# Optimization experiments

Measured on AMD Instinct MI355X. Metric: run time of the kernel, lower is better.

Reference implementation:

```python
import jax, jax.numpy as jnp
import numpy as np

N_NODES, N_EDGES, BATCH = 50000, 100000, 256
H = 64            # dim_hidden_features
D_NODE, D_EDGE, D_RBF = 110, 8, 8
D_SET = 2 * H     # Set2Set input_dim = 128, output_dim = 256
D_HID = 512
D_CAT = 54
MP_STEPS, S2S_ITERS = 4, 3


def setup_inputs() -> dict:
    key = jax.random.key(0)
    ks = iter(jax.random.split(key, 48))

    def nrm(shape, s=0.05):
        return jax.random.normal(next(ks), shape, dtype=jnp.float32) * s

    inp = {}
    inp["node_attribute"] = jax.random.normal(next(ks), (N_NODES, D_NODE), dtype=jnp.float32)
    inp["edge_attribute"] = jax.random.normal(next(ks), (N_EDGES, D_EDGE), dtype=jnp.float32)
    inp["edge_length"] = jax.random.uniform(next(ks), (N_EDGES,), dtype=jnp.float32)
    inp["src"] = jax.random.randint(next(ks), (N_EDGES,), 0, N_NODES, dtype=jnp.int32)
    inp["dst"] = jax.random.randint(next(ks), (N_EDGES,), 0, N_NODES, dtype=jnp.int32)
    inp["node_graph"] = jnp.sort(jax.random.randint(next(ks), (N_NODES,), 0, BATCH, dtype=jnp.int32))
    # atom_feature_projector
    inp["proj_W"] = nrm((D_NODE, H)); inp["proj_b"] = jnp.zeros((H,), jnp.float32)
    # RBF layer: centers ~ U(0,1), beta = 10 (per reset_parameters)
    inp["centers"] = jax.random.uniform(next(ks), (D_RBF,), dtype=jnp.float32)
    inp["beta"] = jnp.full((D_RBF,), 10.0, jnp.float32)
    # NNConv edge function: Linear(16 -> 64*64), plus NNConv bias
    inp["bond_W"] = nrm((D_EDGE + D_RBF, H * H)); inp["bond_b"] = jnp.zeros((H * H,), jnp.float32)
    inp["conv_b"] = jnp.zeros((H,), jnp.float32)
    # GRU (input H, hidden H); PyTorch layout (3H, in)
    inp["gru_Wih"] = nrm((3 * H, H)); inp["gru_Whh"] = nrm((3 * H, H))
    inp["gru_bih"] = jnp.zeros((3 * H,), jnp.float32); inp["gru_bhh"] = jnp.zeros((3 * H,), jnp.float32)
    # Set2Set LSTM: input 2*D_SET=256, hidden D_SET=128, 2 layers; PyTorch layout (4H, in)
    inp["lstm_Wih0"] = nrm((4 * D_SET, 2 * D_SET)); inp["lstm_Whh0"] = nrm((4 * D_SET, D_SET))
    inp["lstm_bih0"] = jnp.zeros((4 * D_SET,), jnp.float32); inp["lstm_bhh0"] = jnp.zeros((4 * D_SET,), jnp.float32)
    inp["lstm_Wih1"] = nrm((4 * D_SET, D_SET)); inp["lstm_Whh1"] = nrm((4 * D_SET, D_SET))
    inp["lstm_bih1"] = jnp.zeros((4 * D_SET,), jnp.float32); inp["lstm_bhh1"] = jnp.zeros((4 * D_SET,), jnp.float32)
    # sparsify: Linear(256 -> 512) + PReLU(init 0.25)
    inp["sp_W"] = nrm((2 * D_SET, D_HID)); inp["sp_b"] = jnp.zeros((D_HID,), jnp.float32)
    inp["prelu_a"] = jnp.array([0.25], jnp.float32)
    # catalyst1 head: hiddens[0] (512->512 ReLU, 512->512 Tanh) then outputs[0] (512->54)
    inp["h0_W1"] = nrm((D_HID, D_HID)); inp["h0_b1"] = jnp.zeros((D_HID,), jnp.float32)
    inp["h0_W2"] = nrm((D_HID, D_HID)); inp["h0_b2"] = jnp.zeros((D_HID,), jnp.float32)
    inp["out_W"] = nrm((D_HID, D_CAT)); inp["out_b"] = jnp.zeros((D_CAT,), jnp.float32)
    return inp


def _lstm_cell(x, h, c, Wih, Whh, bih, bhh):
    # PyTorch LSTM gate order: i, f, g, o
    g = x @ Wih.T + bih + h @ Whh.T + bhh
    i, f, gg, o = jnp.split(g, 4, axis=-1)
    c = jax.nn.sigmoid(f) * c + jax.nn.sigmoid(i) * jnp.tanh(gg)
    h = jax.nn.sigmoid(o) * jnp.tanh(c)
    return h, c


def reference(node_attribute, edge_attribute, edge_length, src, dst, node_graph,
              proj_W, proj_b, centers, beta, bond_W, bond_b, conv_b,
              gru_Wih, gru_Whh, gru_bih, gru_bhh,
              lstm_Wih0, lstm_Whh0, lstm_bih0, lstm_bhh0,
              lstm_Wih1, lstm_Whh1, lstm_bih1, lstm_bhh1,
              sp_W, sp_b, prelu_a, h0_W1, h0_b1, h0_W2, h0_b2, out_W, out_b):
    n_nodes = node_attribute.shape[0]
    # atom feature projection
    x = jax.nn.relu(node_attribute @ proj_W + proj_b)                       # (N, H)
    # edge features = [edge_attribute, RBF(length)]
    rbf = jnp.exp(-beta * (edge_length[:, None] - centers[None, :]) ** 2)   # (E, 8)
    efeat = jnp.concatenate([edge_attribute, rbf], axis=-1)                 # (E, 16)
    # NNConv per-edge weight matrix; edge features are constant over MP steps
    W_e = (efeat @ bond_W + bond_b).reshape(-1, H, H)                       # (E, H, H)

    feat, h = x, x
    for _ in range(MP_STEPS):
        # NNConv: message = h_src @ W_e, sum-aggregated at dst, plus bias
        m = jnp.einsum('ei,eio->eo', feat[src], W_e)                        # (E, H)
        agg = jax.ops.segment_sum(m, dst, num_segments=n_nodes) + conv_b    # (N, H)
        gx = jax.nn.relu(agg)
        # GRU cell (PyTorch gate order r, z, n)
        gi = gx @ gru_Wih.T + gru_bih
        gh = h @ gru_Whh.T + gru_bhh
        i_r, i_z, i_n = jnp.split(gi, 3, axis=-1)
        h_r, h_z, h_n = jnp.split(gh, 3, axis=-1)
        r = jax.nn.sigmoid(i_r + h_r)
        z = jax.nn.sigmoid(i_z + h_z)
        n = jnp.tanh(i_n + r * h_n)
        h = (1.0 - z) * n + z * h
        feat = h
    node_agg = jnp.concatenate([feat, x], axis=-1)                          # (N, 2H)

    # Set2Set pooling over graphs (segment softmax attention, 2-layer LSTM)
    B = BATCH
    h0 = c0 = jnp.zeros((B, D_SET), node_agg.dtype)
    h1 = c1 = jnp.zeros((B, D_SET), node_agg.dtype)
    q_star = jnp.zeros((B, 2 * D_SET), node_agg.dtype)
    for _ in range(S2S_ITERS):
        h0, c0 = _lstm_cell(q_star, h0, c0, lstm_Wih0, lstm_Whh0, lstm_bih0, lstm_bhh0)
        h1, c1 = _lstm_cell(h0, h1, c1, lstm_Wih1, lstm_Whh1, lstm_bih1, lstm_bhh1)
        q = h1                                                              # (B, 128)
        e = jnp.sum(node_agg * q[node_graph], axis=-1)                      # (N,)
        emax = jax.ops.segment_max(e, node_graph, num_segments=B)
        p = jnp.exp(e - emax[node_graph])
        denom = jax.ops.segment_sum(p, node_graph, num_segments=B)
        alpha = p / denom[node_graph]                                       # per-graph softmax
        r_out = jax.ops.segment_sum(node_agg * alpha[:, None], node_graph, num_segments=B)
        q_star = jnp.concatenate([q, r_out], axis=-1)                       # (B, 256)

    # sparsify (Linear + PReLU)
    feats = q_star @ sp_W + sp_b                                            # (B, 512)
    feats = jnp.where(feats >= 0, feats, prelu_a * feats)
    # catalyst1 head
    hid = jnp.tanh(jax.nn.relu(feats @ h0_W1 + h0_b1) @ h0_W2 + h0_b2)
    return jax.nn.softmax(hid @ out_W + out_b, axis=-1)                     # (B, 54)
```

## Files before the change

kernel.cpp:

```cpp
#include <hip/hip_runtime.h>
#include <math.h>

constexpr int N = 50000;
constexpr int E = 100000;
constexpr int B = 256;
constexpr int H = 64;
constexpr int DN = 110;

#define DEV __device__ __forceinline__

typedef __attribute__((ext_vector_type(8))) short short8;
typedef __attribute__((ext_vector_type(4))) float floatx4;

DEV float sigf(float x) { return 1.0f / (1.0f + expf(-x)); }

DEV short f2bf(float f) {
    unsigned u = __float_as_uint(f);
    unsigned r = (u + 0x7fffu + ((u >> 16) & 1u)) >> 16;
    return (short)r;
}
DEV float bf2f(short s) { return __uint_as_float(((unsigned)(unsigned short)s) << 16); }

DEV void cvt8(const float* p, short8& hi, short8& lo) {
    float4 u0 = *(const float4*)p;
    float4 u1 = *(const float4*)(p + 4);
    float vv[8] = {u0.x, u0.y, u0.z, u0.w, u1.x, u1.y, u1.z, u1.w};
#pragma unroll
    for (int j = 0; j < 8; ++j) {
        short hb = f2bf(vv[j]);
        hi[j] = hb;
        lo[j] = f2bf(vv[j] - bf2f(hb));
    }
}

__global__ void k_izero(int* p, int n) {
    int i = blockIdx.x * 256 + threadIdx.x;
    if (i < n) p[i] = 0;
}

DEV void d_transpose(const float* in, float* out, int R, int C, int idx) {
    int r = idx / C, c = idx % C;
    out[c * R + r] = in[idx];
}

DEV void d_prepB(const float* __restrict__ W, short* __restrict__ out,
                 int NT16, int ld, int trans, int ocap, int idx) {
    int lane = idx & 63;
    int t = idx >> 6;
    int ntile = t % NT16;
    int kt = t / NT16;
    int quad = lane >> 4, col = lane & 15;
    int o = ntile * 16 + col;
    short hi[8], lo[8];
#pragma unroll
    for (int j = 0; j < 8; ++j) {
        int k = kt * 32 + quad * 8 + j;
        float v = 0.0f;
        if (o < ocap) v = trans ? W[(size_t)o * ld + k] : W[(size_t)k * ld + o];
        short hb = f2bf(v);
        hi[j] = hb;
        lo[j] = f2bf(v - bf2f(hb));
    }
    short* dh = out + (((size_t)(t * 2 + 0) * 64 + lane) * 8);
    short* dl = out + (((size_t)(t * 2 + 1) * 64 + lane) * 8);
#pragma unroll
    for (int j = 0; j < 8; ++j) { dh[j] = hi[j]; dl[j] = lo[j]; }
}

DEV void d_prepW(const float* __restrict__ bond_W, const float* __restrict__ bond_b,
                 short* __restrict__ wf, int idx) {
    int lane = idx & 63;
    int t = idx >> 6;
    int ks = t & 1;
    int nt = (t >> 1) & 3;
    int kk = t >> 3;
    const float* S = (kk < 16) ? (bond_W + kk * 4096) : bond_b;
    int quad = lane >> 4, col = lane & 15;
    short hi[8], lo[8];
#pragma unroll
    for (int j = 0; j < 8; ++j) {
        int i = ks * 32 + quad * 8 + j;
        float v = S[i * 64 + nt * 16 + col];
        short hb = f2bf(v);
        hi[j] = hb;
        lo[j] = f2bf(v - bf2f(hb));
    }
    short* dh = wf + (((size_t)(t * 2 + 0) * 64 + lane) * 8);
    short* dl = wf + (((size_t)(t * 2 + 1) * 64 + lane) * 8);
#pragma unroll
    for (int j = 0; j < 8; ++j) { dh[j] = hi[j]; dl[j] = lo[j]; }
}

__launch_bounds__(256)
__global__ void k_prep0(const float* lWih0, const float* lWhh0, const float* lWih1, const float* lWhh1,
                        float* lW0T, float* lU0T, float* lW1T, float* lU1T,
                        const float* bond_W, const float* bond_b, short* wf,
                        const float* gru_Wih, const float* gru_Whh, short* fgI, short* fgH,
                        float* zreg) {
    int idx = blockIdx.x * 256 + threadIdx.x;
    if (idx < 131072) { d_transpose(lWih0, lW0T, 512, 256, idx); return; }
    idx -= 131072;
    if (idx < 65536) { d_transpose(lWhh0, lU0T, 512, 128, idx); return; }
    idx -= 65536;
    if (idx < 65536) { d_transpose(lWih1, lW1T, 512, 128, idx); return; }
    idx -= 65536;
    if (idx < 65536) { d_transpose(lWhh1, lU1T, 512, 128, idx); return; }
    idx -= 65536;
    if (idx < 8704) { d_prepW(bond_W, bond_b, wf, idx); return; }
    idx -= 8704;
    if (idx < 1536) { d_prepB(gru_Wih, fgI, 12, 64, 1, 192, idx); return; }
    idx -= 1536;
    if (idx < 1536) { d_prepB(gru_Whh, fgH, 12, 64, 1, 192, idx); return; }
    idx -= 1536;
    if (idx < 196608) { zreg[idx] = 0.0f; return; }
}
constexpr int PREP0_TOTAL = 131072 + 3 * 65536 + 8704 + 2 * 1536 + 196608;

__launch_bounds__(256)
__global__ void k_prephead(const float* sp_W, short* fsp, const float* h0_W1, short* fw1,
                           const float* h0_W2, short* fw2, const float* out_W, short* fow) {
    int idx = blockIdx.x * 256 + threadIdx.x;
    if (idx < 16384) { d_prepB(sp_W, fsp, 32, 512, 0, 512, idx); return; }
    idx -= 16384;
    if (idx < 32768) { d_prepB(h0_W1, fw1, 32, 512, 0, 512, idx); return; }
    idx -= 32768;
    if (idx < 32768) { d_prepB(h0_W2, fw2, 32, 512, 0, 512, idx); return; }
    idx -= 32768;
    if (idx < 4096) { d_prepB(out_W, fow, 4, 54, 0, 54, idx); return; }
}
constexpr int PREPH_TOTAL = 16384 + 2 * 32768 + 4096;

__global__ void k_deg(const int* __restrict__ dst, int* __restrict__ deg) {
    int e = blockIdx.x * 256 + threadIdx.x;
    if (e < E) atomicAdd(&deg[dst[e]], 1);
}
__global__ void k_scan1(const int* __restrict__ deg, int* __restrict__ bsum) {
    __shared__ int s[256];
    int b = blockIdx.x, tid = threadIdx.x;
    int idx = b * 256 + tid;
    s[tid] = (idx < N) ? deg[idx] : 0;
    __syncthreads();
    for (int st = 128; st > 0; st >>= 1) {
        if (tid < st) s[tid] += s[tid + st];
        __syncthreads();
    }
    if (tid == 0) bsum[b] = s[0];
}
__global__ void k_scan2p(int* __restrict__ bsum, int nb) {
    __shared__ int s[256];
    int tid = threadIdx.x;
    int v = (tid < nb) ? bsum[tid] : 0;
    s[tid] = v;
    __syncthreads();
    for (int off = 1; off < 256; off <<= 1) {
        int t = (tid >= off) ? s[tid - off] : 0;
        __syncthreads();
        s[tid] += t;
        __syncthreads();
    }
    if (tid < nb) bsum[tid] = s[tid] - v;
}
__global__ void k_scan3(const int* __restrict__ deg, const int* __restrict__ bsum,
                        int* __restrict__ cursor, int* __restrict__ roff) {
    __shared__ int s[256];
    int b = blockIdx.x, tid = threadIdx.x;
    int idx = b * 256 + tid;
    int v = (idx < N) ? deg[idx] : 0;
    s[tid] = v;
    __syncthreads();
    for (int off = 1; off < 256; off <<= 1) {
        int t = (tid >= off) ? s[tid - off] : 0;
        __syncthreads();
        s[tid] += t;
        __syncthreads();
    }
    if (idx < N) {
        int start = bsum[b] + s[tid] - v;
        cursor[idx] = start;
        roff[idx] = start;
    }
    if (idx == 0) roff[N] = E;
}
__global__ void k_scat(const int* __restrict__ src, const int* __restrict__ dst,
                       int* __restrict__ cursor, int* __restrict__ srcp,
                       int* __restrict__ epos) {
    int e = blockIdx.x * 256 + threadIdx.x;
    if (e >= E) return;
    int d = dst[e];
    int pos = atomicAdd(&cursor[d], 1);
    srcp[pos] = src[e];
    epos[e] = pos;
}

__launch_bounds__(256)
__global__ void k_proj(const float* __restrict__ na, const float* __restrict__ W,
                       const float* __restrict__ b, float* __restrict__ x,
                       short* __restrict__ hs) {
    __shared__ float Ws[DN * 64];
    __shared__ float as[16][112];
    int tid = threadIdx.x;
    for (int i = tid; i < DN * 64; i += 256) Ws[i] = W[i];
    int n0 = blockIdx.x * 16;
    for (int i = tid; i < 16 * DN; i += 256) {
        int nn = i / DN, ii = i % DN;
        as[nn][ii] = na[(n0 + nn) * DN + ii];
    }
    __syncthreads();
    int o = tid & 63, ng = tid >> 6;
    float bo = b[o];
    for (int j = 0; j < 4; ++j) {
        int nn = ng * 4 + j;
        float acc = bo;
#pragma unroll 10
        for (int i = 0; i < DN; ++i) acc += as[nn][i] * Ws[i * 64 + o];
        float v = fmaxf(acc, 0.0f);
        int n = n0 + nn;
        x[(size_t)n * 64 + o] = v;
        short hb = f2bf(v);
        hs[(size_t)n * 128 + o] = hb;
        hs[(size_t)n * 128 + 64 + o] = f2bf(v - bf2f(hb));
    }
}

__global__ void k_efeat2(const float* __restrict__ ea, const float* __restrict__ el,
                         const float* __restrict__ centers, const float* __restrict__ beta,
                         const int* __restrict__ epos, float* __restrict__ ef_t) {
    int e = blockIdx.x * 256 + threadIdx.x;
    if (e >= E) return;
    int pos = epos[e];
    float L = el[e];
#pragma unroll
    for (int j = 0; j < 8; ++j) ef_t[j * E + pos] = ea[e * 8 + j];
#pragma unroll
    for (int j = 0; j < 8; ++j) {
        float d = L - centers[j];
        ef_t[(8 + j) * E + pos] = expf(-beta[j] * d * d);
    }
    ef_t[16 * E + pos] = 1.0f;
}

__launch_bounds__(256)
__global__ void k_msg8(const short* __restrict__ hs, const float* __restrict__ ef_t,
                       const short* __restrict__ wf, const int* __restrict__ srcp,
                       float* __restrict__ m) {
    __shared__ float efs[17 * 64];
    __shared__ int srcs[64];

    int tid = threadIdx.x;
    int e0 = blockIdx.x * 64;
    int lane = tid & 63;
    int nt = tid >> 6;
    int quad = lane >> 4, col = lane & 15;

    if (tid < 64) {
        int eg = e0 + tid;
        srcs[tid] = (eg < E) ? srcp[eg] : 0;
    }
    for (int i = tid; i < 17 * 64; i += 256) {
        int kk = i >> 6, e = i & 63;
        int eg = e0 + e;
        efs[i] = (eg < E) ? ef_t[(size_t)kk * E + eg] : 0.0f;
    }
    __syncthreads();

    short8 Ah[4][2], Al[4][2];
#pragma unroll
    for (int mt = 0; mt < 4; ++mt) {
        int s = srcs[mt * 16 + col];
        const short* hp = hs + (size_t)s * 128 + quad * 8;
#pragma unroll
        for (int ks = 0; ks < 2; ++ks) {
            Ah[mt][ks] = *(const short8*)(hp + ks * 32);
            Al[mt][ks] = *(const short8*)(hp + 64 + ks * 32);
        }
    }

    const short8* Wf = (const short8*)wf;
    float C[4][4] = {};

#define LOADB(d0, d1, d2, d3, KK)                      \
    {                                                  \
        int tb_ = ((KK) * 4 + nt) * 2;                 \
        d0 = Wf[((tb_ + 0) * 2 + 0) * 64 + lane];      \
        d1 = Wf[((tb_ + 1) * 2 + 0) * 64 + lane];      \
        d2 = Wf[((tb_ + 0) * 2 + 1) * 64 + lane];      \
        d3 = Wf[((tb_ + 1) * 2 + 1) * 64 + lane];      \
    }

    short8 c0, c1, c2, c3, n0_, n1_, n2_, n3_, q0, q1, q2, q3;
    LOADB(c0, c1, c2, c3, 0);
    LOADB(n0_, n1_, n2_, n3_, 1);
    LOADB(q0, q1, q2, q3, 2);

#pragma unroll 1
    for (int kk = 0; kk < 17; ++kk) {
        int kn = kk + 3;
        if (kn > 16) kn = 16;
        short8 p0, p1, p2, p3;
        LOADB(p0, p1, p2, p3, kn);

#pragma unroll
        for (int mt = 0; mt < 4; ++mt) {
            floatx4 T = {0.0f, 0.0f, 0.0f, 0.0f};
            T = __builtin_amdgcn_mfma_f32_16x16x32_bf16(Ah[mt][0], c0, T, 0, 0, 0);
            T = __builtin_amdgcn_mfma_f32_16x16x32_bf16(Ah[mt][1], c1, T, 0, 0, 0);
            T = __builtin_amdgcn_mfma_f32_16x16x32_bf16(Al[mt][0], c0, T, 0, 0, 0);
            T = __builtin_amdgcn_mfma_f32_16x16x32_bf16(Al[mt][1], c1, T, 0, 0, 0);
            T = __builtin_amdgcn_mfma_f32_16x16x32_bf16(Ah[mt][0], c2, T, 0, 0, 0);
            T = __builtin_amdgcn_mfma_f32_16x16x32_bf16(Ah[mt][1], c3, T, 0, 0, 0);
            float4 ef = *(const float4*)&efs[kk * 64 + mt * 16 + quad * 4];
            C[mt][0] += ef.x * T[0];
            C[mt][1] += ef.y * T[1];
            C[mt][2] += ef.z * T[2];
            C[mt][3] += ef.w * T[3];
        }
        c0 = n0_; c1 = n1_; c2 = n2_; c3 = n3_;
        n0_ = q0; n1_ = q1; n2_ = q2; n3_ = q3;
        q0 = p0; q1 = p1; q2 = p2; q3 = p3;
    }
#undef LOADB

    int o = nt * 16 + col;
#pragma unroll
    for (int mt = 0; mt < 4; ++mt) {
#pragma unroll
        for (int r = 0; r < 4; ++r) {
            int eg = e0 + mt * 16 + quad * 4 + r;
            if (eg < E) m[(size_t)eg * 64 + o] = C[mt][r];
        }
    }
}

__launch_bounds__(256)
__global__ void k_gru3(const float* __restrict__ m, const int* __restrict__ roff,
                       const float* __restrict__ conv_b, short* __restrict__ hs,
                       const short* __restrict__ fI, const short* __restrict__ fH,
                       const float* __restrict__ bih, const float* __restrict__ bhh) {
    int tid = threadIdx.x, lane = tid & 63, nt = tid >> 6;
    int quad = lane >> 4, col = lane & 15;
    int n0 = blockIdx.x * 32;

    short8 Gh[2][2], Gl[2][2], Hh[2][2], Hl[2][2];
#pragma unroll
    for (int mt = 0; mt < 2; ++mt) {
        int node = n0 + mt * 16 + col;
        bool ok = node < N;
        int nc = ok ? node : (N - 1);
        int rs = roff[nc];
        int re = ok ? roff[nc + 1] : rs;
        float acc[2][8];
#pragma unroll
        for (int ks = 0; ks < 2; ++ks) {
            const float* cb = conv_b + ks * 32 + quad * 8;
#pragma unroll
            for (int j = 0; j < 8; ++j) acc[ks][j] = cb[j];
        }
        for (int r = rs; r < re; ++r) {
            const float* mp = m + (size_t)r * 64 + quad * 8;
            float4 a0 = *(const float4*)mp;
            float4 a1 = *(const float4*)(mp + 4);
            float4 b0 = *(const float4*)(mp + 32);
            float4 b1 = *(const float4*)(mp + 36);
            acc[0][0] += a0.x; acc[0][1] += a0.y; acc[0][2] += a0.z; acc[0][3] += a0.w;
            acc[0][4] += a1.x; acc[0][5] += a1.y; acc[0][6] += a1.z; acc[0][7] += a1.w;
            acc[1][0] += b0.x; acc[1][1] += b0.y; acc[1][2] += b0.z; acc[1][3] += b0.w;
            acc[1][4] += b1.x; acc[1][5] += b1.y; acc[1][6] += b1.z; acc[1][7] += b1.w;
        }
        const short* hp = hs + (size_t)nc * 128 + quad * 8;
#pragma unroll
        for (int ks = 0; ks < 2; ++ks) {
            short8 hh8 = *(const short8*)(hp + ks * 32);
            short8 hl8 = *(const short8*)(hp + 64 + ks * 32);
            Hh[mt][ks] = hh8;
            Hl[mt][ks] = hl8;
#pragma unroll
            for (int j = 0; j < 8; ++j) {
                float g = ok ? fmaxf(acc[ks][j], 0.0f) : 0.0f;
                short gb = f2bf(g);
                Gh[mt][ks][j] = gb;
                Gl[mt][ks][j] = f2bf(g - bf2f(gb));
            }
        }
        if (!ok) {
#pragma unroll
            for (int ks = 0; ks < 2; ++ks) {
                Hh[mt][ks] = short8{0,0,0,0,0,0,0,0};
                Hl[mt][ks] = short8{0,0,0,0,0,0,0,0};
            }
        }
    }
    __syncthreads();

    const short8* FI = (const short8*)fI;
    const short8* FH = (const short8*)fH;
    floatx4 aI[2][3] = {}, aH[2][3] = {};
#pragma unroll
    for (int ks = 0; ks < 2; ++ks) {
        short8 bIh[3], bIl[3], bHh[3], bHl[3];
#pragma unroll
        for (int g = 0; g < 3; ++g) {
            int t = ks * 12 + g * 4 + nt;
            bIh[g] = FI[(t * 2 + 0) * 64 + lane];
            bIl[g] = FI[(t * 2 + 1) * 64 + lane];
            bHh[g] = FH[(t * 2 + 0) * 64 + lane];
            bHl[g] = FH[(t * 2 + 1) * 64 + lane];
        }
#pragma unroll
        for (int mt = 0; mt < 2; ++mt) {
#pragma unroll
            for (int g = 0; g < 3; ++g) {
                aI[mt][g] = __builtin_amdgcn_mfma_f32_16x16x32_bf16(Gh[mt][ks], bIh[g], aI[mt][g], 0, 0, 0);
                aI[mt][g] = __builtin_amdgcn_mfma_f32_16x16x32_bf16(Gl[mt][ks], bIh[g], aI[mt][g], 0, 0, 0);
                aI[mt][g] = __builtin_amdgcn_mfma_f32_16x16x32_bf16(Gh[mt][ks], bIl[g], aI[mt][g], 0, 0, 0);
                aH[mt][g] = __builtin_amdgcn_mfma_f32_16x16x32_bf16(Hh[mt][ks], bHh[g], aH[mt][g], 0, 0, 0);
                aH[mt][g] = __builtin_amdgcn_mfma_f32_16x16x32_bf16(Hl[mt][ks], bHh[g], aH[mt][g], 0, 0, 0);
                aH[mt][g] = __builtin_amdgcn_mfma_f32_16x16x32_bf16(Hh[mt][ks], bHl[g], aH[mt][g], 0, 0, 0);
            }
        }
    }

    int o = nt * 16 + col;
    float br = bih[o], bz = bih[64 + o], bn = bih[128 + o];
    float cr = bhh[o], cz = bhh[64 + o], cn = bhh[128 + o];
#pragma unroll
    for (int mt = 0; mt < 2; ++mt) {
#pragma unroll
        for (int r = 0; r < 4; ++r) {
            int node = n0 + mt * 16 + quad * 4 + r;
            if (node >= N) continue;
            float rg = sigf(aI[mt][0][r] + br + aH[mt][0][r] + cr);
            float z  = sigf(aI[mt][1][r] + bz + aH[mt][1][r] + cz);
            float ng = tanhf(aI[mt][2][r] + bn + rg * (aH[mt][2][r] + cn));
            size_t hb_ = (size_t)node * 128 + o;
            float hold = bf2f(hs[hb_]) + bf2f(hs[hb_ + 64]);
            float hn = (1.0f - z) * ng + z * hold;
            short hi = f2bf(hn);
            hs[hb_] = hi;
            hs[hb_ + 64] = f2bf(hn - bf2f(hi));
        }
    }
}

__global__ void k_bounds2(const int* __restrict__ ng, int* __restrict__ gs, int* __restrict__ ge) {
    int n = blockIdx.x * 256 + threadIdx.x;
    if (n >= N) return;
    int g = ng[n];
    int gp = (n == 0) ? -1 : ng[n - 1];
    if (g != gp) {
        gs[g] = n;
        if (n > 0) ge[gp] = n;
        for (int q = gp + 1; q < g; ++q) { gs[q] = 0; ge[q] = 0; }
    }
    if (n == N - 1) {
        ge[g] = N;
        for (int q = g + 1; q < B; ++q) { gs[q] = 0; ge[q] = 0; }
    }
}

__launch_bounds__(256)
__global__ void k_s2s(float* __restrict__ h0, float* __restrict__ c0,
                      float* __restrict__ h1, float* __restrict__ c1,
                      float* __restrict__ q_star,
                      const float* __restrict__ W0T, const float* __restrict__ U0T,
                      const float* __restrict__ b0i, const float* __restrict__ b0h,
                      const float* __restrict__ W1T, const float* __restrict__ U1T,
                      const float* __restrict__ b1i, const float* __restrict__ b1h,
                      const short* __restrict__ hs, const float* __restrict__ x,
                      const int* __restrict__ gs, const int* __restrict__ ge) {
    __shared__ float xb[256], hb[128], gb[512], h0n[128], qv[128];
    __shared__ float mrg[4][2][64];
    __shared__ float ml[4][2];
    int g = blockIdx.x, tid = threadIdx.x;
    xb[tid] = q_star[g * 256 + tid];
    if (tid < 128) hb[tid] = h0[g * 128 + tid];
    __syncthreads();
    float g0 = b0i[tid] + b0h[tid];
    float g1 = b0i[tid + 256] + b0h[tid + 256];
    for (int i = 0; i < 256; ++i) {
        float xx = xb[i];
        g0 += xx * W0T[i * 512 + tid];
        g1 += xx * W0T[i * 512 + tid + 256];
    }
    for (int i = 0; i < 128; ++i) {
        float hh = hb[i];
        g0 += hh * U0T[i * 512 + tid];
        g1 += hh * U0T[i * 512 + tid + 256];
    }
    gb[tid] = g0; gb[tid + 256] = g1;
    __syncthreads();
    if (tid < 128) {
        float ii = gb[tid], ff = gb[128 + tid], gg = gb[256 + tid], oo = gb[384 + tid];
        float c = sigf(ff) * c0[g * 128 + tid] + sigf(ii) * tanhf(gg);
        float hn = sigf(oo) * tanhf(c);
        c0[g * 128 + tid] = c; h0[g * 128 + tid] = hn; h0n[tid] = hn;
        hb[tid] = h1[g * 128 + tid];
    }
    __syncthreads();
    float ga = b1i[tid] + b1h[tid];
    float gbv = b1i[tid + 256] + b1h[tid + 256];
    for (int i = 0; i < 128; ++i) {
        float xx = h0n[i], hh = hb[i];
        ga  += xx * W1T[i * 512 + tid]       + hh * U1T[i * 512 + tid];
        gbv += xx * W1T[i * 512 + tid + 256] + hh * U1T[i * 512 + tid + 256];
    }
    gb[tid] = ga; gb[tid + 256] = gbv;
    __syncthreads();
    if (tid < 128) {
        float ii = gb[tid], ff = gb[128 + tid], gg = gb[256 + tid], oo = gb[384 + tid];
        float c = sigf(ff) * c1[g * 128 + tid] + sigf(ii) * tanhf(gg);
        float hn = sigf(oo) * tanhf(c);
        c1[g * 128 + tid] = c; h1[g * 128 + tid] = hn;
        q_star[g * 256 + tid] = hn;
        qv[tid] = hn;
    }
    __syncthreads();
    int s0v = gs[g], s1v = ge[g];
    int lane = tid & 63, grp = tid >> 6;
    float qh = qv[lane], qx = qv[64 + lane];
    float mM = -INFINITY, lL = 0.0f, nh = 0.0f, nx = 0.0f;
    for (int n = s0v + grp; n < s1v; n += 16) {
        float hv[4], xv[4], e[4];
#pragma unroll
// ... 86 lines not shown
    __shared__ float sm[16][64];
    __shared__ float smax[16], sinv[16];
    int tid = threadIdx.x, lane = tid & 63, nt = tid >> 6;
    int quad = lane >> 4, col = lane & 15;
    int s0 = blockIdx.x * 16;
    const short8* F = (const short8*)Bf;
    floatx4 T = {0.0f, 0.0f, 0.0f, 0.0f};
    const float* ap = A + (size_t)(s0 + col) * 512 + quad * 8;
#pragma unroll 4
    for (int kt = 0; kt < 16; ++kt) {
        short8 ah, al;
        cvt8(ap + kt * 32, ah, al);
        int t = kt * 4 + nt;
        short8 bh = F[(t * 2 + 0) * 64 + lane];
        short8 bl = F[(t * 2 + 1) * 64 + lane];
        T = __builtin_amdgcn_mfma_f32_16x16x32_bf16(ah, bh, T, 0, 0, 0);
        T = __builtin_amdgcn_mfma_f32_16x16x32_bf16(al, bh, T, 0, 0, 0);
        T = __builtin_amdgcn_mfma_f32_16x16x32_bf16(ah, bl, T, 0, 0, 0);
    }
    int o = nt * 16 + col;
    float b = (o < 54) ? ob[o] : 0.0f;
#pragma unroll
    for (int r = 0; r < 4; ++r)
        sm[quad * 4 + r][o] = (o < 54) ? (T[r] + b) : -1e30f;
    __syncthreads();
    if (tid < 16) {
        float m = -INFINITY;
        for (int j = 0; j < 54; ++j) m = fmaxf(m, sm[tid][j]);
        float s = 0.0f;
        for (int j = 0; j < 54; ++j) s += expf(sm[tid][j] - m);
        smax[tid] = m;
        sinv[tid] = 1.0f / s;
    }
    __syncthreads();
    for (int idx = tid; idx < 16 * 54; idx += 256) {
        int srow = idx / 54, oo = idx % 54;
        out[(size_t)(s0 + srow) * 54 + oo] = expf(sm[srow][oo] - smax[srow]) * sinv[srow];
    }
}

extern "C" void kernel_launch(void* const* d_in, const int* in_sizes, int n_in,
                              void* d_out, int out_size, void* d_ws, size_t ws_size,
                              hipStream_t stream) {
    const float* node_attr = (const float*)d_in[0];
    const float* edge_attr = (const float*)d_in[1];
    const float* edge_len  = (const float*)d_in[2];
    const int*   src       = (const int*)d_in[3];
    const int*   dst       = (const int*)d_in[4];
    const int*   node_grph = (const int*)d_in[5];
    const float* proj_W    = (const float*)d_in[6];
    const float* proj_b    = (const float*)d_in[7];
    const float* centers   = (const float*)d_in[8];
    const float* beta      = (const float*)d_in[9];
    const float* bond_W    = (const float*)d_in[10];
    const float* bond_b    = (const float*)d_in[11];
    const float* conv_b    = (const float*)d_in[12];
    const float* gru_Wih   = (const float*)d_in[13];
    const float* gru_Whh   = (const float*)d_in[14];
    const float* gru_bih   = (const float*)d_in[15];
    const float* gru_bhh   = (const float*)d_in[16];
    const float* lWih0     = (const float*)d_in[17];
    const float* lWhh0     = (const float*)d_in[18];
    const float* lbih0     = (const float*)d_in[19];
    const float* lbhh0     = (const float*)d_in[20];
    const float* lWih1     = (const float*)d_in[21];
    const float* lWhh1     = (const float*)d_in[22];
    const float* lbih1     = (const float*)d_in[23];
    const float* lbhh1     = (const float*)d_in[24];
    const float* sp_W      = (const float*)d_in[25];
    const float* sp_b      = (const float*)d_in[26];
    const float* prelu_a   = (const float*)d_in[27];
    const float* h0_W1     = (const float*)d_in[28];
    const float* h0_b1     = (const float*)d_in[29];
    const float* h0_W2     = (const float*)d_in[30];
    const float* h0_b2     = (const float*)d_in[31];
    const float* out_W     = (const float*)d_in[32];
    const float* out_b     = (const float*)d_in[33];
    float* out = (float*)d_out;

    float* ws = (float*)d_ws;
    size_t off = 0;
    float* x      = ws + off; off += (size_t)N * 64;
    float* hsf    = ws + off; off += (size_t)N * 64;
    float* ef_t   = ws + off; off += (size_t)E * 17;
    float* m      = ws + off; off += (size_t)E * 64;
    float* wfrag  = ws + off; off += 17 * 16 * 64 * 8 / 2;
    float* fgI    = ws + off; off += 2 * 64 * 192 / 2;
    float* fgH    = ws + off; off += 2 * 64 * 192 / 2;
    float* lW0T   = ws + off; off += 256 * 512;
    float* lU0T   = ws + off; off += 128 * 512;
    float* lW1T   = ws + off; off += 128 * 512;
    float* lU1T   = ws + off; off += 128 * 512;
    float* h0     = ws + off; off += B * 128;
    float* c0     = ws + off; off += B * 128;
    float* h1     = ws + off; off += B * 128;
    float* c1     = ws + off; off += B * 128;
    float* q_star = ws + off; off += B * 256;
    int* gs       = (int*)(ws + off); off += B;
    int* ge       = (int*)(ws + off); off += B;
    int* deg      = (int*)(ws + off); off += N;
    int* cursor   = (int*)(ws + off); off += N;
    int* roff     = (int*)(ws + off); off += N + 1;
    int* bsum     = (int*)(ws + off); off += 256;
    int* srcp     = (int*)(ws + off); off += E;
    int* epos     = (int*)(ws + off); off += E;

    short* hs = (short*)hsf;

    short* fsp = (short*)ef_t;
    short* fw1 = (short*)(ef_t + 131072);
    short* fw2 = (short*)(ef_t + 131072 + 262144);
    short* fow = (short*)(ef_t + 131072 + 2 * 262144);
    float* hb1 = ef_t + 131072 + 2 * 262144 + 32768;
    float* hb2 = hb1 + 131072;

    constexpr int NB = (N + 255) / 256;

    k_izero<<<NB, 256, 0, stream>>>(deg, N);
    k_deg<<<(E + 255) / 256, 256, 0, stream>>>(dst, deg);
    k_scan1<<<NB, 256, 0, stream>>>(deg, bsum);
    k_scan2p<<<1, 256, 0, stream>>>(bsum, NB);
    k_scan3<<<NB, 256, 0, stream>>>(deg, bsum, cursor, roff);
    k_scat<<<(E + 255) / 256, 256, 0, stream>>>(src, dst, cursor, srcp, epos);

    k_prep0<<<(PREP0_TOTAL + 255) / 256, 256, 0, stream>>>(
        lWih0, lWhh0, lWih1, lWhh1, lW0T, lU0T, lW1T, lU1T,
        bond_W, bond_b, (short*)wfrag, gru_Wih, gru_Whh, (short*)fgI, (short*)fgH, h0);

    k_proj<<<N / 16, 256, 0, stream>>>(node_attr, proj_W, proj_b, x, hs);
    k_efeat2<<<(E + 255) / 256, 256, 0, stream>>>(edge_attr, edge_len, centers, beta, epos, ef_t);

    k_bounds2<<<(N + 255) / 256, 256, 0, stream>>>(node_grph, gs, ge);

    for (int step = 0; step < 4; ++step) {
        k_msg8<<<(E + 63) / 64, 256, 0, stream>>>(hs, ef_t, (const short*)wfrag, srcp, m);
        k_gru3<<<(N + 31) / 32, 256, 0, stream>>>(m, roff, conv_b, hs,
                                                  (const short*)fgI, (const short*)fgH,
                                                  gru_bih, gru_bhh);
    }

    k_prephead<<<(PREPH_TOTAL + 255) / 256, 256, 0, stream>>>(
        sp_W, fsp, h0_W1, fw1, h0_W2, fw2, out_W, fow);

    for (int it = 0; it < 3; ++it) {
        k_s2s<<<B, 256, 0, stream>>>(h0, c0, h1, c1, q_star,
                                     lW0T, lU0T, lbih0, lbhh0,
                                     lW1T, lU1T, lbih1, lbhh1,
                                     hs, x, gs, ge);
    }

    k_hgemm<0><<<dim3(16, 8), 256, 0, stream>>>(q_star, fsp, sp_b, prelu_a, hb1, 256, 32);
    k_hgemm<1><<<dim3(16, 8), 256, 0, stream>>>(hb1, fw1, h0_b1, nullptr, hb2, 512, 32);
    k_hgemm<2><<<dim3(16, 8), 256, 0, stream>>>(hb2, fw2, h0_b2, nullptr, hb1, 512, 32);
    k_hout<<<16, 256, 0, stream>>>(hb1, fow, out_b, out);
}
```

Measured before the change: 781.8 us.

## Reorder NNConv as per-node aggregation of edge-feature outer products, fused with GRU

The message step now first accumulates, per destination node, the outer product of edge features (17) with source hidden states (64), then multiplies that 16x1088 matrix by the bond weight tensor with MFMA, and runs the GRU in the same kernel. This removes the per-edge 64-wide message buffer and the separate GRU kernel, and reduces the GEMM from edges to nodes. Hidden state is ping-ponged between two buffers, edge features move to a row-major 20-float layout, and the node projection becomes an MFMA kernel with a new kcap bound in the weight prep. The cost is a serial per-lane edge gather loop holding 68 float accumulators per thread plus a large shared-memory tile, which may limit occupancy.

New measurement: 984.7 us. 26.0% more time.

```diff
diff --git a/kernel.cpp b/kernel.cpp
--- a/kernel.cpp
+++ b/kernel.cpp
@@ -11,6 +11,7 @@
 
 typedef __attribute__((ext_vector_type(8))) short short8;
 typedef __attribute__((ext_vector_type(4))) float floatx4;
+typedef __attribute__((ext_vector_type(4))) unsigned uint4v;
 
 DEV float sigf(float x) { return 1.0f / (1.0f + expf(-x)); }
 
@@ -21,16 +22,44 @@
 }
 DEV float bf2f(short s) { return __uint_as_float(((unsigned)(unsigned short)s) << 16); }
 
+DEV unsigned cvtpk(float a, float b) {
+    unsigned r;
+    asm("v_cvt_pk_bf16_f32 %0, %1, %2" : "=v"(r) : "v"(a), "v"(b));
+    return r;
+}
+DEV void split2(float f0, float f1, unsigned& hp, unsigned& lp) {
+    hp = cvtpk(f0, f1);
+    float f0p = __uint_as_float(hp << 16);
+    float f1p = __uint_as_float(hp & 0xffff0000u);
+    lp = cvtpk(f0 - f0p, f1 - f1p);
+}
+DEV void readA(const unsigned* ap, short8& hi, short8& lo) {
+    uint4v a0 = *(const uint4v*)ap;
+    uint4v a1 = *(const uint4v*)(ap + 4);
+    union { unsigned u[4]; short8 s; } Hu, Lu;
+    Hu.u[0] = __builtin_amdgcn_perm(a0[1], a0[0], 0x05040100u);
+    Lu.u[0] = __builtin_amdgcn_perm(a0[1], a0[0], 0x07060302u);
+    Hu.u[1] = __builtin_amdgcn_perm(a0[3], a0[2], 0x05040100u);
+    Lu.u[1] = __builtin_amdgcn_perm(a0[3], a0[2], 0x07060302u);
+    Hu.u[2] = __builtin_amdgcn_perm(a1[1], a1[0], 0x05040100u);
+    Lu.u[2] = __builtin_amdgcn_perm(a1[1], a1[0], 0x07060302u);
+    Hu.u[3] = __builtin_amdgcn_perm(a1[3], a1[2], 0x05040100u);
+    Lu.u[3] = __builtin_amdgcn_perm(a1[3], a1[2], 0x07060302u);
+    hi = Hu.s; lo = Lu.s;
+}
+DEV void splitf8(float4 v0, float4 v1, short8& hi, short8& lo) {
+    union { unsigned u[4]; short8 s; } Hu, Lu;
+    split2(v0.x, v0.y, Hu.u[0], Lu.u[0]);
+    split2(v0.z, v0.w, Hu.u[1], Lu.u[1]);
+    split2(v1.x, v1.y, Hu.u[2], Lu.u[2]);
+    split2(v1.z, v1.w, Hu.u[3], Lu.u[3]);
+    hi = Hu.s; lo = Lu.s;
+}
+
 DEV void cvt8(const float* p, short8& hi, short8& lo) {
     float4 u0 = *(const float4*)p;
     float4 u1 = *(const float4*)(p + 4);
-    float vv[8] = {u0.x, u0.y, u0.z, u0.w, u1.x, u1.y, u1.z, u1.w};
-#pragma unroll
-    for (int j = 0; j < 8; ++j) {
-        short hb = f2bf(vv[j]);
-        hi[j] = hb;
-        lo[j] = f2bf(vv[j] - bf2f(hb));
-    }
+    splitf8(u0, u1, hi, lo);
 }
 
 __global__ void k_izero(int* p, int n) {
@@ -44,7 +73,7 @@
 }
 
 DEV void d_prepB(const float* __restrict__ W, short* __restrict__ out,
-                 int NT16, int ld, int trans, int ocap, int idx) {
+                 int NT16, int ld, int trans, int ocap, int kcap, int idx) {
     int lane = idx & 63;
     int t = idx >> 6;
     int ntile = t % NT16;
@@ -56,7 +85,7 @@
     for (int j = 0; j < 8; ++j) {
         int k = kt * 32 + quad * 8 + j;
         float v = 0.0f;
-        if (o < ocap) v = trans ? W[(size_t)o * ld + k] : W[(size_t)k * ld + o];
+        if (o < ocap && k < kcap) v = trans ? W[(size_t)o * ld + k] : W[(size_t)k * ld + o];
         short hb = f2bf(v);
         hi[j] = hb;
         lo[j] = f2bf(v - bf2f(hb));
@@ -96,6 +125,7 @@
                         float* lW0T, float* lU0T, float* lW1T, float* lU1T,
                         const float* bond_W, const float* bond_b, short* wf,
                         const float* gru_Wih, const float* gru_Whh, short* fgI, short* fgH,
+                        const float* proj_W, short* fproj,
                         float* zreg) {
     int idx = blockIdx.x * 256 + threadIdx.x;
     if (idx < 131072) { d_transpose(lWih0, lW0T, 512, 256, idx); return; }
@@ -108,25 +138,27 @@
     idx -= 65536;
     if (idx < 8704) { d_prepW(bond_W, bond_b, wf, idx); return; }
     idx -= 8704;
-    if (idx < 1536) { d_prepB(gru_Wih, fgI, 12, 64, 1, 192, idx); return; }
+    if (idx < 1536) { d_prepB(gru_Wih, fgI, 12, 64, 1, 192, 64, idx); return; }
     idx -= 1536;
-    if (idx < 1536) { d_prepB(gru_Whh, fgH, 12, 64, 1, 192, idx); return; }
+    if (idx < 1536) { d_prepB(gru_Whh, fgH, 12, 64, 1, 192, 64, idx); return; }
     idx -= 1536;
+    if (idx < 1024) { d_prepB(proj_W, fproj, 4, 64, 0, 64, DN, idx); return; }
+    idx -= 1024;
     if (idx < 196608) { zreg[idx] = 0.0f; return; }
 }
-constexpr int PREP0_TOTAL = 131072 + 3 * 65536 + 8704 + 2 * 1536 + 196608;
+constexpr int PREP0_TOTAL = 131072 + 3 * 65536 + 8704 + 2 * 1536 + 1024 + 196608;
 
 __launch_bounds__(256)
 __global__ void k_prephead(const float* sp_W, short* fsp, const float* h0_W1, short* fw1,
                            const float* h0_W2, short* fw2, const float* out_W, short* fow) {
     int idx = blockIdx.x * 256 + threadIdx.x;
-    if (idx < 16384) { d_prepB(sp_W, fsp, 32, 512, 0, 512, idx); return; }
+    if (idx < 16384) { d_prepB(sp_W, fsp, 32, 512, 0, 512, 256, idx); return; }
     idx -= 16384;
-    if (idx < 32768) { d_prepB(h0_W1, fw1, 32, 512, 0, 512, idx); return; }
+    if (idx < 32768) { d_prepB(h0_W1, fw1, 32, 512, 0, 512, 512, idx); return; }
     idx -= 32768;
-    if (idx < 32768) { d_prepB(h0_W2, fw2, 32, 512, 0, 512, idx); return; }
+    if (idx < 32768) { d_prepB(h0_W2, fw2, 32, 512, 0, 512, 512, idx); return; }
     idx -= 32768;
-    if (idx < 4096) { d_prepB(out_W, fow, 4, 54, 0, 54, idx); return; }
+    if (idx < 4096) { d_prepB(out_W, fow, 4, 54, 0, 54, 512, idx); return; }
 }
 constexpr int PREPH_TOTAL = 16384 + 2 * 32768 + 4096;
 
@@ -193,28 +225,48 @@
 }
 
 __launch_bounds__(256)
-__global__ void k_proj(const float* __restrict__ na, const float* __restrict__ W,
-                       const float* __restrict__ b, float* __restrict__ x,
-                       short* __restrict__ hs) {
-    __shared__ float Ws[DN * 64];
-    __shared__ float as[16][112];
-    int tid = threadIdx.x;
-    for (int i = tid; i < DN * 64; i += 256) Ws[i] = W[i];
-    int n0 = blockIdx.x * 16;
+__global__ void k_projm(const float* __restrict__ na, const short* __restrict__ fp,
+                        const float* __restrict__ b, float* __restrict__ x,
+                        short* __restrict__ hs) {
+    __shared__ float as[16 * 132];
+    int tid = threadIdx.x, lane = tid & 63, nt = tid >> 6;
+    int quad = lane >> 4, col = lane & 15;
+    int s0 = blockIdx.x * 16;
     for (int i = tid; i < 16 * DN; i += 256) {
-        int nn = i / DN, ii = i % DN;
-        as[nn][ii] = na[(n0 + nn) * DN + ii];
-    }
-    __syncthreads();
-    int o = tid & 63, ng = tid >> 6;
+        int r = i / DN, c = i % DN;
+        as[r * 132 + c] = na[(size_t)s0 * DN + i];
+    }
+    for (int i = tid; i < 16 * 22; i += 256) {
+        int r = i / 22, c = DN + i % 22;
+        as[r * 132 + c] = 0.0f;
+    }
+    __syncthreads();
+    const short8* F = (const short8*)fp;
+    floatx4 T = {0.0f, 0.0f, 0.0f, 0.0f};
+#pragma unroll
+    for (int kt = 0; kt < 4; ++kt) {
+        const float* ap = as + col * 132 + kt * 32 + quad * 8;
+        short8 ah, al;
+#pragma unroll
+        for (int j = 0; j < 8; ++j) {
+            float v = ap[j];
+            short hb = f2bf(v);
+            ah[j] = hb;
+            al[j] = f2bf(v - bf2f(hb));
+        }
+        int t = kt * 4 + nt;
+        short8 bh = F[(t * 2 + 0) * 64 + lane];
+        short8 bl = F[(t * 2 + 1) * 64 + lane];
+        T = __builtin_amdgcn_mfma_f32_16x16x32_bf16(ah, bh, T, 0, 0, 0);
+        T = __builtin_amdgcn_mfma_f32_16x16x32_bf16(al, bh, T, 0, 0, 0);
+        T = __builtin_amdgcn_mfma_f32_16x16x32_bf16(ah, bl, T, 0, 0, 0);
+    }
+    int o = nt * 16 + col;
     float bo = b[o];
-    for (int j = 0; j < 4; ++j) {
-        int nn = ng * 4 + j;
-        float acc = bo;
-#pragma unroll 10
-        for (int i = 0; i < DN; ++i) acc += as[nn][i] * Ws[i * 64 + o];
-        float v = fmaxf(acc, 0.0f);
-        int n = n0 + nn;
+#pragma unroll
+    for (int r = 0; r < 4; ++r) {
+        int n = s0 + quad * 4 + r;
+        float v = fmaxf(T[r] + bo, 0.0f);
         x[(size_t)n * 64 + o] = v;
         short hb = f2bf(v);
         hs[(size_t)n * 128 + o] = hb;
@@ -224,220 +276,164 @@
 
 __global__ void k_efeat2(const float* __restrict__ ea, const float* __restrict__ el,
                          const float* __restrict__ centers, const float* __restrict__ beta,
-                         const int* __restrict__ epos, float* __restrict__ ef_t) {
+                         const int* __restrict__ epos, float* __restrict__ ef2) {
     int e = blockIdx.x * 256 + threadIdx.x;
     if (e >= E) return;
     int pos = epos[e];
     float L = el[e];
-#pragma unroll
-    for (int j = 0; j < 8; ++j) ef_t[j * E + pos] = ea[e * 8 + j];
+    float* o = ef2 + (size_t)pos * 20;
+#pragma unroll
+    for (int j = 0; j < 8; ++j) o[j] = ea[e * 8 + j];
 #pragma unroll
     for (int j = 0; j < 8; ++j) {
         float d = L - centers[j];
-        ef_t[(8 + j) * E + pos] = expf(-beta[j] * d * d);
-    }
-    ef_t[16 * E + pos] = 1.0f;
+        o[8 + j] = expf(-beta[j] * d * d);
+    }
+    o[16] = 1.0f;
 }
 
 __launch_bounds__(256)
-__global__ void k_msg8(const short* __restrict__ hs, const float* __restrict__ ef_t,
-                       const short* __restrict__ wf, const int* __restrict__ srcp,
-                       float* __restrict__ m) {
-    __shared__ float efs[17 * 64];
-    __shared__ int srcs[64];
-
-    int tid = threadIdx.x;
-    int e0 = blockIdx.x * 64;
-    int lane = tid & 63;
-    int nt = tid >> 6;
+__global__ void k_mp(const short* __restrict__ hs_in, short* __restrict__ hs_out,
+                     const float* __restrict__ ef2, const short* __restrict__ wf,
+                     const int* __restrict__ roff, const int* __restrict__ srcp,
+                     const float* __restrict__ conv_b,
+                     const short* __restrict__ fI, const short* __restrict__ fH,
+                     const float* __restrict__ bih, const float* __restrict__ bhh) {
+    __shared__ unsigned G2[16][1089];
+    __shared__ float Gr[16][65];
+
+    int tid = threadIdx.x, lane = tid & 63, w = tid >> 6;
     int quad = lane >> 4, col = lane & 15;
-
-    if (tid < 64) {
-        int eg = e0 + tid;
-        srcs[tid] = (eg < E) ? srcp[eg] : 0;
-    }
-    for (int i = tid; i < 17 * 64; i += 256) {
-        int kk = i >> 6, e = i & 63;
-        int eg = e0 + e;
-        efs[i] = (eg < E) ? ef_t[(size_t)kk * E + eg] : 0.0f;
-    }
-    __syncthreads();
-
-    short8 Ah[4][2], Al[4][2];
-#pragma unroll
-    for (int mt = 0; mt < 4; ++mt) {
-        int s = srcs[mt * 16 + col];
-        const short* hp = hs + (size_t)s * 128 + quad * 8;
+    int n0 = blockIdx.x * 16;
+
+    float g[4][17];
+#pragma unroll
+    for (int j = 0; j < 4; ++j)
+#pragma unroll
+        for (int kk = 0; kk < 17; ++kk) g[j][kk] = 0.0f;
+
+#pragma unroll
+    for (int j = 0; j < 4; ++j) {
+        int node = n0 + w * 4 + j;
+        int rs = roff[node], re = roff[node + 1];
+        for (int r = rs; r < re; ++r) {
+            int s = srcp[r];
+            float fv = bf2f(hs_in[(size_t)s * 128 + lane]) +
+                       bf2f(hs_in[(size_t)s * 128 + 64 + lane]);
+            const float* ep = ef2 + (size_t)r * 20;
+#pragma unroll
+            for (int kk = 0; kk < 17; ++kk) g[j][kk] += ep[kk] * fv;
+        }
+    }
+#pragma unroll
+    for (int j = 0; j < 4; ++j) {
+        int row = w * 4 + j;
+#pragma unroll
+        for (int k2 = 0; k2 < 8; ++k2) {
+            unsigned hp, lp;
+            split2(g[j][2 * k2], g[j][2 * k2 + 1], hp, lp);
+            G2[row][(2 * k2) * 64 + lane]     = __builtin_amdgcn_perm(lp, hp, 0x05040100u);
+            G2[row][(2 * k2 + 1) * 64 + lane] = __builtin_amdgcn_perm(lp, hp, 0x07060302u);
+        }
+        unsigned hp, lp;
+        split2(g[j][16], 0.0f, hp, lp);
+        G2[row][16 * 64 + lane] = __builtin_amdgcn_perm(lp, hp, 0x05040100u);
+    }
+    __syncthreads();
+
+    const short8* Wf = (const short8*)wf;
+    floatx4 Cc = {0.0f, 0.0f, 0.0f, 0.0f};
+
+#define LOADW(dh, dl, KTT)                                     \
+    {                                                          \
+        int kk_ = (KTT) >> 1, ks_ = (KTT) & 1;                 \
+        int t_ = (kk_ * 4 + w) * 2 + ks_;                      \
+        dh = Wf[(t_ * 2 + 0) * 64 + lane];                     \
+        dl = Wf[(t_ * 2 + 1) * 64 + lane];                     \
+    }
+    short8 Bh0, Bl0, Bh1, Bl1;
+    LOADW(Bh0, Bl0, 0);
+    LOADW(Bh1, Bl1, 1);
+#pragma unroll 1
+    for (int ktt = 0; ktt < 34; ++ktt) {
+        int kn = ktt + 2; if (kn > 33) kn = 33;
+        short8 Ph, Pl;
+        LOADW(Ph, Pl, kn);
+        int kk = ktt >> 1, ks = ktt & 1;
+        short8 ah, al;
+        readA(&G2[col][kk * 64 + ks * 32 + quad * 8], ah, al);
+        Cc = __builtin_amdgcn_mfma_f32_16x16x32_bf16(ah, Bh0, Cc, 0, 0, 0);
+        Cc = __builtin_amdgcn_mfma_f32_16x16x32_bf16(al, Bh0, Cc, 0, 0, 0);
+        Cc = __builtin_amdgcn_mfma_f32_16x16x32_bf16(ah, Bl0, Cc, 0, 0, 0);
+        Bh0 = Bh1; Bl0 = Bl1; Bh1 = Ph; Bl1 = Pl;
+    }
+#undef LOADW
+
+    {
+        float cb = conv_b[w * 16 + col];
+#pragma unroll
+        for (int r = 0; r < 4; ++r)
+            Gr[quad * 4 + r][w * 16 + col] = fmaxf(Cc[r] + cb, 0.0f);
+    }
+    __syncthreads();
+
+    short8 Gh[2], Gl[2], Hh[2], Hl[2];
+#pragma unroll
+    for (int ks = 0; ks < 2; ++ks) {
+        const float* gp = &Gr[col][ks * 32 + quad * 8];
+        float4 f0 = *(const float4*)gp;
+        float4 f1 = *(const float4*)(gp + 4);
+        splitf8(f0, f1, Gh[ks], Gl[ks]);
+    }
+    {
+        const short* hp = hs_in + (size_t)(n0 + col) * 128 + quad * 8;
 #pragma unroll
         for (int ks = 0; ks < 2; ++ks) {
-            Ah[mt][ks] = *(const short8*)(hp + ks * 32);
-            Al[mt][ks] = *(const short8*)(hp + 64 + ks * 32);
-        }
-    }
-
-    const short8* Wf = (const short8*)wf;
-    float C[4][4] = {};
-
-#define LOADB(d0, d1, d2, d3, KK)                      \
-    {                                                  \
-        int tb_ = ((KK) * 4 + nt) * 2;                 \
-        d0 = Wf[((tb_ + 0) * 2 + 0) * 64 + lane];      \
-        d1 = Wf[((tb_ + 1) * 2 + 0) * 64 + lane];      \
-        d2 = Wf[((tb_ + 0) * 2 + 1) * 64 + lane];      \
-        d3 = Wf[((tb_ + 1) * 2 + 1) * 64 + lane];      \
-    }
-
-    short8 c0, c1, c2, c3, n0_, n1_, n2_, n3_, q0, q1, q2, q3;
-    LOADB(c0, c1, c2, c3, 0);
-    LOADB(n0_, n1_, n2_, n3_, 1);
-    LOADB(q0, q1, q2, q3, 2);
-
-#pragma unroll 1
-    for (int kk = 0; kk < 17; ++kk) {
-        int kn = kk + 3;
-        if (kn > 16) kn = 16;
-        short8 p0, p1, p2, p3;
-        LOADB(p0, p1, p2, p3, kn);
-
-#pragma unroll
-        for (int mt = 0; mt < 4; ++mt) {
-            floatx4 T = {0.0f, 0.0f, 0.0f, 0.0f};
-            T = __builtin_amdgcn_mfma_f32_16x16x32_bf16(Ah[mt][0], c0, T, 0, 0, 0);
-            T = __builtin_amdgcn_mfma_f32_16x16x32_bf16(Ah[mt][1], c1, T, 0, 0, 0);
-            T = __builtin_amdgcn_mfma_f32_16x16x32_bf16(Al[mt][0], c0, T, 0, 0, 0);
-            T = __builtin_amdgcn_mfma_f32_16x16x32_bf16(Al[mt][1], c1, T, 0, 0, 0);
-            T = __builtin_amdgcn_mfma_f32_16x16x32_bf16(Ah[mt][0], c2, T, 0, 0, 0);
-            T = __builtin_amdgcn_mfma_f32_16x16x32_bf16(Ah[mt][1], c3, T, 0, 0, 0);
-            float4 ef = *(const float4*)&efs[kk * 64 + mt * 16 + quad * 4];
-            C[mt][0] += ef.x * T[0];
-            C[mt][1] += ef.y * T[1];
-            C[mt][2] += ef.z * T[2];
-            C[mt][3] += ef.w * T[3];
-        }
-        c0 = n0_; c1 = n1_; c2 = n2_; c3 = n3_;
-        n0_ = q0; n1_ = q1; n2_ = q2; n3_ = q3;
-        q0 = p0; q1 = p1; q2 = p2; q3 = p3;
-    }
-#undef LOADB
-
-    int o = nt * 16 + col;
-#pragma unroll
-    for (int mt = 0; mt < 4; ++mt) {
-#pragma unroll
-        for (int r = 0; r < 4; ++r) {
-            int eg = e0 + mt * 16 + quad * 4 + r;
-            if (eg < E) m[(size_t)eg * 64 + o] = C[mt][r];
-        }
-    }
-}
-
-__launch_bounds__(256)
-__global__ void k_gru3(const float* __restrict__ m, const int* __restrict__ roff,
-                       const float* __restrict__ conv_b, short* __restrict__ hs,
-                       const short* __restrict__ fI, const short* __restrict__ fH,
-                       const float* __restrict__ bih, const float* __restrict__ bhh) {
-    int tid = threadIdx.x, lane = tid & 63, nt = tid >> 6;
-    int quad = lane >> 4, col = lane & 15;
-    int n0 = blockIdx.x * 32;
-
-    short8 Gh[2][2], Gl[2][2], Hh[2][2], Hl[2][2];
-#pragma unroll
-    for (int mt = 0; mt < 2; ++mt) {
-        int node = n0 + mt * 16 + col;
-        bool ok = node < N;
-        int nc = ok ? node : (N - 1);
-        int rs = roff[nc];
-        int re = ok ? roff[nc + 1] : rs;
-        float acc[2][8];
-#pragma unroll
-        for (int ks = 0; ks < 2; ++ks) {
-            const float* cb = conv_b + ks * 32 + quad * 8;
-#pragma unroll
-            for (int j = 0; j < 8; ++j) acc[ks][j] = cb[j];
-        }
-        for (int r = rs; r < re; ++r) {
-            const float* mp = m + (size_t)r * 64 + quad * 8;
-            float4 a0 = *(const float4*)mp;
-            float4 a1 = *(const float4*)(mp + 4);
-            float4 b0 = *(const float4*)(mp + 32);
-            float4 b1 = *(const float4*)(mp + 36);
-            acc[0][0] += a0.x; acc[0][1] += a0.y; acc[0][2] += a0.z; acc[0][3] += a0.w;
-            acc[0][4] += a1.x; acc[0][5] += a1.y; acc[0][6] += a1.z; acc[0][7] += a1.w;
-            acc[1][0] += b0.x; acc[1][1] += b0.y; acc[1][2] += b0.z; acc[1][3] += b0.w;
-            acc[1][4] += b1.x; acc[1][5] += b1.y; acc[1][6] += b1.z; acc[1][7] += b1.w;
-        }
-        const short* hp = hs + (size_t)nc * 128 + quad * 8;
-#pragma unroll
-        for (int ks = 0; ks < 2; ++ks) {
-            short8 hh8 = *(const short8*)(hp + ks * 32);
-            short8 hl8 = *(const short8*)(hp + 64 + ks * 32);
-            Hh[mt][ks] = hh8;
-            Hl[mt][ks] = hl8;
-#pragma unroll
-            for (int j = 0; j < 8; ++j) {
-                float g = ok ? fmaxf(acc[ks][j], 0.0f) : 0.0f;
-                short gb = f2bf(g);
-                Gh[mt][ks][j] = gb;
-                Gl[mt][ks][j] = f2bf(g - bf2f(gb));
-            }
-        }
-        if (!ok) {
-#pragma unroll
-            for (int ks = 0; ks < 2; ++ks) {
-                Hh[mt][ks] = short8{0,0,0,0,0,0,0,0};
-                Hl[mt][ks] = short8{0,0,0,0,0,0,0,0};
-            }
-        }
-    }
-    __syncthreads();
+            Hh[ks] = *(const short8*)(hp + ks * 32);
+            Hl[ks] = *(const short8*)(hp + 64 + ks * 32);
+        }
+    }
 
     const short8* FI = (const short8*)fI;
     const short8* FH = (const short8*)fH;
-    floatx4 aI[2][3] = {}, aH[2][3] = {};
+    floatx4 aI[3] = {}, aH[3] = {};
 #pragma unroll
     for (int ks = 0; ks < 2; ++ks) {
         short8 bIh[3], bIl[3], bHh[3], bHl[3];
 #pragma unroll
-        for (int g = 0; g < 3; ++g) {
-            int t = ks * 12 + g * 4 + nt;
-            bIh[g] = FI[(t * 2 + 0) * 64 + lane];
-            bIl[g] = FI[(t * 2 + 1) * 64 + lane];
-            bHh[g] = FH[(t * 2 + 0) * 64 + lane];
-            bHl[g] = FH[(t * 2 + 1) * 64 + lane];
-        }
-#pragma unroll
-        for (int mt = 0; mt < 2; ++mt) {
-#pragma unroll
-            for (int g = 0; g < 3; ++g) {
-                aI[mt][g] = __builtin_amdgcn_mfma_f32_16x16x32_bf16(Gh[mt][ks], bIh[g], aI[mt][g], 0, 0, 0);
-                aI[mt][g] = __builtin_amdgcn_mfma_f32_16x16x32_bf16(Gl[mt][ks], bIh[g], aI[mt][g], 0, 0, 0);
-                aI[mt][g] = __builtin_amdgcn_mfma_f32_16x16x32_bf16(Gh[mt][ks], bIl[g], aI[mt][g], 0, 0, 0);
-                aH[mt][g] = __builtin_amdgcn_mfma_f32_16x16x32_bf16(Hh[mt][ks], bHh[g], aH[mt][g], 0, 0, 0);
-                aH[mt][g] = __builtin_amdgcn_mfma_f32_16x16x32_bf16(Hl[mt][ks], bHh[g], aH[mt][g], 0, 0, 0);
-                aH[mt][g] = __builtin_amdgcn_mfma_f32_16x16x32_bf16(Hh[mt][ks], bHl[g], aH[mt][g], 0, 0, 0);
-            }
-        }
-    }
-
-    int o = nt * 16 + col;
+        for (int g2 = 0; g2 < 3; ++g2) {
+            int t = ks * 12 + g2 * 4 + w;
+            bIh[g2] = FI[(t * 2 + 0) * 64 + lane];
+            bIl[g2] = FI[(t * 2 + 1) * 64 + lane];
+            bHh[g2] = FH[(t * 2 + 0) * 64 + lane];
+            bHl[g2] = FH[(t * 2 + 1) * 64 + lane];
+        }
+#pragma unroll
+        for (int g2 = 0; g2 < 3; ++g2) {
+            aI[g2] = __builtin_amdgcn_mfma_f32_16x16x32_bf16(Gh[ks], bIh[g2], aI[g2], 0, 0, 0);
+            aI[g2] = __builtin_amdgcn_mfma_f32_16x16x32_bf16(Gl[ks], bIh[g2], aI[g2], 0, 0, 0);
+            aI[g2] = __builtin_amdgcn_mfma_f32_16x16x32_bf16(Gh[ks], bIl[g2], aI[g2], 0, 0, 0);
+            aH[g2] = __builtin_amdgcn_mfma_f32_16x16x32_bf16(Hh[ks], bHh[g2], aH[g2], 0, 0, 0);
+            aH[g2] = __builtin_amdgcn_mfma_f32_16x16x32_bf16(Hl[ks], bHh[g2], aH[g2], 0, 0, 0);
+            aH[g2] = __builtin_amdgcn_mfma_f32_16x16x32_bf16(Hh[ks], bHl[g2], aH[g2], 0, 0, 0);
+        }
+    }
+
+    int o = w * 16 + col;
     float br = bih[o], bz = bih[64 + o], bn = bih[128 + o];
     float cr = bhh[o], cz = bhh[64 + o], cn = bhh[128 + o];
 #pragma unroll
-    for (int mt = 0; mt < 2; ++mt) {
-#pragma unroll
-        for (int r = 0; r < 4; ++r) {
-            int node = n0 + mt * 16 + quad * 4 + r;
-            if (node >= N) continue;
-            float rg = sigf(aI[mt][0][r] + br + aH[mt][0][r] + cr);
-            float z  = sigf(aI[mt][1][r] + bz + aH[mt][1][r] + cz);
-            float ng = tanhf(aI[mt][2][r] + bn + rg * (aH[mt][2][r] + cn));
-            size_t hb_ = (size_t)node * 128 + o;
-            float hold = bf2f(hs[hb_]) + bf2f(hs[hb_ + 64]);
-            float hn = (1.0f - z) * ng + z * hold;
-            short hi = f2bf(hn);
-            hs[hb_] = hi;
-            hs[hb_ + 64] = f2bf(hn - bf2f(hi));
-        }
+    for (int r = 0; r < 4; ++r) {
+        int node = n0 + quad * 4 + r;
+        float rg = sigf(aI[0][r] + br + aH[0][r] + cr);
+        float z  = sigf(aI[1][r] + bz + aH[1][r] + cz);
+        float ng = tanhf(aI[2][r] + bn + rg * (aH[2][r] + cn));
+        size_t hb_ = (size_t)node * 128 + o;
+        float hold = bf2f(hs_in[hb_]) + bf2f(hs_in[hb_ + 64]);
+        float hn = (1.0f - z) * ng + z * hold;
+        short hi2 = f2bf(hn);
+        hs_out[hb_] = hi2;
+        hs_out[hb_ + 64] = f2bf(hn - bf2f(hi2));
     }
 }
 
@@ -690,11 +686,12 @@
     size_t off = 0;
     float* x      = ws + off; off += (size_t)N * 64;
     float* hsf    = ws + off; off += (size_t)N * 64;
-    float* ef_t   = ws + off; off += (size_t)E * 17;
-    float* m      = ws + off; off += (size_t)E * 64;
+    float* hs1f   = ws + off; off += (size_t)N * 64;
+    float* ef2    = ws + off; off += (size_t)E * 20;
     float* wfrag  = ws + off; off += 17 * 16 * 64 * 8 / 2;
     float* fgI    = ws + off; off += 2 * 64 * 192 / 2;
     float* fgH    = ws + off; off += 2 * 64 * 192 / 2;
+    float* fproj  = ws + off; off += 16 * 1024 / 2;
     float* lW0T   = ws + off; off += 256 * 512;
     float* lU0T   = ws + off; off += 128 * 512;
     float* lW1T   = ws + off; off += 128 * 512;
@@ -713,13 +710,14 @@
     int* srcp     = (int*)(ws + off); off += E;
     int* epos     = (int*)(ws + off); off += E;
 
-    short* hs = (short*)hsf;
-
-    short* fsp = (short*)ef_t;
-    short* fw1 = (short*)(ef_t + 131072);
-    short* fw2 = (short*)(ef_t + 131072 + 262144);
-    short* fow = (short*)(ef_t + 131072 + 2 * 262144);
-    float* hb1 = ef_t + 131072 + 2 * 262144 + 32768;
+    short* hsA = (short*)hsf;
+    short* hsB = (short*)hs1f;
+
+    short* fsp = (short*)ef2;
+    short* fw1 = (short*)(ef2 + 131072);
+    short* fw2 = (short*)(ef2 + 131072 + 262144);
+    short* fow = (short*)(ef2 + 131072 + 2 * 262144);
+    float* hb1 = ef2 + 131072 + 2 * 262144 + 32768;
     float* hb2 = hb1 + 131072;
 
     constexpr int NB = (N + 255) / 256;
@@ -733,18 +731,19 @@
 
     k_prep0<<<(PREP0_TOTAL + 255) / 256, 256, 0, stream>>>(
         lWih0, lWhh0, lWih1, lWhh1, lW0T, lU0T, lW1T, lU1T,
-        bond_W, bond_b, (short*)wfrag, gru_Wih, gru_Whh, (short*)fgI, (short*)fgH, h0);
-
-    k_proj<<<N / 16, 256, 0, stream>>>(node_attr, proj_W, proj_b, x, hs);
-    k_efeat2<<<(E + 255) / 256, 256, 0, stream>>>(edge_attr, edge_len, centers, beta, epos, ef_t);
+        bond_W, bond_b, (short*)wfrag, gru_Wih, gru_Whh, (short*)fgI, (short*)fgH,
+        proj_W, (short*)fproj, h0);
+
+    k_projm<<<N / 16, 256, 0, stream>>>(node_attr, (const short*)fproj, proj_b, x, hsA);
+    k_efeat2<<<(E + 255) / 256, 256, 0, stream>>>(edge_attr, edge_len, centers, beta, epos, ef2);
 
     k_bounds2<<<(N + 255) / 256, 256, 0, stream>>>(node_grph, gs, ge);
 
     for (int step = 0; step < 4; ++step) {
-        k_msg8<<<(E + 63) / 64, 256, 0, stream>>>(hs, ef_t, (const short*)wfrag, srcp, m);
-        k_gru3<<<(N + 31) / 32, 256, 0, stream>>>(m, roff, conv_b, hs,
-                                                  (const short*)fgI, (const short*)fgH,
-                                                  gru_bih, gru_bhh);
+        k_mp<<<N / 16, 256, 0, stream>>>(hsA, hsB, ef2, (const short*)wfrag, roff, srcp,
+                                         conv_b, (const short*)fgI, (const short*)fgH,
+                                         gru_bih, gru_bhh);
+        short* t = hsA; hsA = hsB; hsB = t;
     }
 
     k_prephead<<<(PREPH_TOTAL + 255) / 256, 256, 0, stream>>>(
@@ -754,7 +753,7 @@
         k_s2s<<<B, 256, 0, stream>>>(h0, c0, h1, c1, q_star,
                                      lW0T, lU0T, lbih0, lbhh0,
                                      lW1T, lU1T, lbih1, lbhh1,
-                                     hs, x, gs, ge);
+                                     hsA, x, gs, ge);
     }
 
     k_hgemm<0><<<dim3(16, 8), 256, 0, stream>>>(q_star, fsp, sp_b, prelu_a, hb1, 256, 32);
```
